# Kernel tuning notes

Hardware: AMD Instinct MI355X
Metric: run time of the kernel (lower is better)

Reference implementation:

```python
import jax, jax.numpy as jnp
import numpy as np

B, S, D_IN, D = 4, 4096, 512, 256


def setup_inputs() -> dict:
    key = jax.random.key(0)
    ks = jax.random.split(key, 7)
    return {
        "query": jax.random.normal(ks[0], (B, S, D_IN), dtype=jnp.float32),
        "key": jax.random.normal(ks[1], (B, S, D_IN), dtype=jnp.float32),
        "value": jax.random.normal(ks[2], (B, S, D), dtype=jnp.float32),
        "Wq": jax.random.normal(ks[3], (D, D_IN), dtype=jnp.float32) * (1.0 / np.sqrt(D_IN)),
        "bq": jax.random.normal(ks[4], (D,), dtype=jnp.float32) * 0.01,
        "Wk": jax.random.normal(ks[5], (D, D_IN), dtype=jnp.float32) * (1.0 / np.sqrt(D_IN)),
        "bk": jax.random.normal(ks[6], (D,), dtype=jnp.float32) * 0.01,
        "scale_factor": jnp.ones((), dtype=jnp.float32),  # source uses scale_factor = 1
        "dropout_p": 0,  # fixed to 0 -> dropout is identity (deterministic baseline)
    }


def reference(query, key, value, Wq, bq, Wk, bk, scale_factor, dropout_p):
    # q/k linear projections: [B,S,512] -> [B,S,256]
    q = jnp.einsum("bsi,di->bsd", query, Wq) + bq
    k = jnp.einsum("bsi,di->bsd", key, Wk) + bk
    # scaled dot-product attention scores [B,S,S]
    scores = jnp.einsum("bqd,bkd->bqk", q, k) * scale_factor
    attn = jax.nn.softmax(scores, axis=-1)
    # dropout_p == 0 -> identity
    out = jnp.einsum("bqk,bkd->bqd", attn, value)
    return out
```

## Files before the change

### kernel.cpp

```cpp
#include <hip/hip_runtime.h>

#define S_LEN 4096
#define NROWS 16384

typedef float f32x4 __attribute__((ext_vector_type(4)));
typedef _Float16 f16x8 __attribute__((ext_vector_type(8)));
typedef _Float16 f16x4 __attribute__((ext_vector_type(4)));

__device__ __forceinline__ unsigned short f2h(float f) {
  _Float16 h = (_Float16)f;
  return __builtin_bit_cast(unsigned short, h);
}

__device__ __forceinline__ float ex2(float x) {
  return __builtin_amdgcn_exp2f(x);
}

__device__ __forceinline__ void gload16(const void* g, void* l) {
  __builtin_amdgcn_global_load_lds(
      (const __attribute__((address_space(1))) void*)g,
      (__attribute__((address_space(3))) void*)l, 16, 0, 0);
}

__global__ void cw_kernel(const float* __restrict__ Wq, const float* __restrict__ Wk,
                          unsigned short* __restrict__ Wqb, unsigned short* __restrict__ Wkb) {
  const int i = (blockIdx.x * 256 + threadIdx.x) * 8;
  if (i >= 131072) return;
  unsigned short tmp[8] __attribute__((aligned(16)));
#pragma unroll
  for (int u = 0; u < 8; ++u) tmp[u] = f2h(Wq[i + u]);
  *(uint4*)(Wqb + i) = ((const uint4*)tmp)[0];
#pragma unroll
  for (int u = 0; u < 8; ++u) tmp[u] = f2h(Wk[i + u]);
  *(uint4*)(Wkb + i) = ((const uint4*)tmp)[0];
}

__global__ __launch_bounds__(256) void vt_kernel(const float* __restrict__ V,
                                                 unsigned short* __restrict__ Vt) {
  __shared__ float tile[64][65];
  const int tid = threadIdx.x;
  const int b = blockIdx.z, s0 = blockIdx.x * 64, d0 = blockIdx.y * 64;
  {
    const int r = tid >> 2, cs = (tid & 3) * 16;
    const float* src = V + ((long)b * S_LEN + s0 + r) * 256 + d0 + cs;
#pragma unroll
    for (int u = 0; u < 4; ++u) {
      const f32x4 v = __builtin_nontemporal_load((const f32x4*)(src + 4 * u));
      tile[r][cs + 4 * u + 0] = v[0]; tile[r][cs + 4 * u + 1] = v[1];
      tile[r][cs + 4 * u + 2] = v[2]; tile[r][cs + 4 * u + 3] = v[3];
    }
  }
  __syncthreads();
  {
    const int d = tid >> 2, ss = (tid & 3) * 16;
    unsigned short tmp[16] __attribute__((aligned(16)));
#pragma unroll
    for (int u = 0; u < 16; ++u) tmp[u] = f2h(tile[ss + u][d]);
    unsigned short* dst = Vt + ((long)b * 256 + d0 + d) * S_LEN + s0 + ss;
    *(uint4*)dst = ((const uint4*)tmp)[0];
    *((uint4*)dst + 1) = ((const uint4*)tmp)[1];
  }
}

__global__ __launch_bounds__(256, 4) void proj_kernel(
    const float* __restrict__ Xq, const float* __restrict__ Xk,
    const unsigned short* __restrict__ Wqb, const unsigned short* __restrict__ Wkb,
    const float* __restrict__ bq, const float* __restrict__ bk,
    unsigned short* __restrict__ Qb, unsigned short* __restrict__ Kb,
    const float* __restrict__ scale_ptr) {
  const int tid = threadIdx.x;
  const int lane = tid & 63, w = tid >> 6;
  const int h = lane >> 4, cc = lane & 15;
  const int z = blockIdx.y;
  const float* X = z ? Xk : Xq;
  const unsigned short* Wb = z ? Wkb : Wqb;
  const float* bias = z ? bk : bq;
  unsigned short* out = z ? Kb : Qb;
  const float sc = z ? 1.f : scale_ptr[0] * 1.44269504088896340736f;
  const int rowbase = blockIdx.x * 64;

  __shared__ char sx[8192];
  __shared__ char sw[32768];

  f32x4 acc[16];
  const f32x4 fz = {0.f, 0.f, 0.f, 0.f};
#pragma unroll
  for (int nf = 0; nf < 16; ++nf) acc[nf] = fz;

  for (int kstep = 0; kstep < 8; ++kstep) {
    const int k0 = kstep * 64;
    __syncthreads();
    {
      const int r = tid >> 2;
      const int cb0 = (tid & 3) * 2;
      const float* src = X + (long)(rowbase + r) * 512 + k0 + (tid & 3) * 16;
      float xv[16];
#pragma unroll
      for (int u = 0; u < 4; ++u) {
        const f32x4 v = __builtin_nontemporal_load((const f32x4*)(src + 4 * u));
        xv[4 * u + 0] = v[0]; xv[4 * u + 1] = v[1];
        xv[4 * u + 2] = v[2]; xv[4 * u + 3] = v[3];
      }
      unsigned short tmp[16] __attribute__((aligned(16)));
#pragma unroll
      for (int u = 0; u < 16; ++u) tmp[u] = f2h(xv[u]);
      *(uint4*)(sx + r * 128 + ((cb0 ^ (r & 7)) * 16)) = ((const uint4*)tmp)[0];
      *(uint4*)(sx + r * 128 + (((cb0 + 1) ^ (r & 7)) * 16)) = ((const uint4*)tmp)[1];
    }
#pragma unroll
    for (int i = 0; i < 8; ++i) {
      const int off = w * 8192 + i * 1024 + lane * 16;
      const int row = off >> 7;
      const int lcb = (lane & 7) ^ (row & 7);
      gload16(Wb + (long)row * 512 + k0 + lcb * 8, sw + w * 8192 + i * 1024);
    }
    __syncthreads();
#pragma unroll
    for (int ks = 0; ks < 2; ++ks) {
      const int rl = 16 * w + cc;
      const f16x8 af = *(const f16x8*)(sx + rl * 128 + (((h + 4 * ks) ^ (rl & 7)) * 16));
#pragma unroll
      for (int nf = 0; nf < 16; ++nf) {
        const int n = cc + 16 * nf;
        const f16x8 bf = *(const f16x8*)(sw + n * 128 + (((h + 4 * ks) ^ (n & 7)) * 16));
        acc[nf] = __builtin_amdgcn_mfma_f32_16x16x32_f16(af, bf, acc[nf], 0, 0, 0);
      }
    }
  }
#pragma unroll
  for (int nf = 0; nf < 16; ++nf) {
    const float bv = bias[cc + 16 * nf];
#pragma unroll
    for (int r = 0; r < 4; ++r) {
      const long grow = rowbase + 16 * w + 4 * h + r;
      out[grow * 256 + cc + 16 * nf] = f2h((acc[nf][r] + bv) * sc);
    }
  }
}

__global__ __launch_bounds__(256, 2) void attn_kernel(
    const unsigned short* __restrict__ Qb, const unsigned short* __restrict__ Kb,
    const unsigned short* __restrict__ Vt, float* __restrict__ out0,
    unsigned short* __restrict__ p16, float2* __restrict__ stats,
    int* __restrict__ cnt, int nsplit, int nchunks) {
  extern __shared__ char smem[];
  const int tid = threadIdx.x;
  const int lane = tid & 63, w = tid >> 6;
  const int h = lane >> 4, c = lane & 15;

  int* s_item_p = (int*)(smem + 69632);
  if (tid == 0) {
    const unsigned x = __builtin_amdgcn_s_getreg(6164) & 7u;
    const int pref = (int)x * nchunks / 8;
    int item = 0;
    for (int k = 0; k < nchunks; ++k) {
      const int ch = (pref + k) % nchunks;
      const int t = atomicAdd(cnt + ch, 1);
      if (t < 32) { item = ch * 32 + t; break; }
    }
    *s_item_p = item;
  }
  __syncthreads();
  const int nid = *s_item_p;
  const int gqt = nid & 255;
  const int split = nid >> 8;

  const int b = gqt >> 6;
  const int qrow0 = (gqt & 63) * 64;
  const long brow = (long)b * S_LEN;

  const int kv_len = S_LEN / nsplit;
  const int kv0 = split * kv_len;
  const int nit = kv_len / 32;

  f16x8 qf[8];
  {
    const unsigned short* qbase = Qb + (brow + qrow0 + w * 16 + c) * 256 + h * 8;
#pragma unroll
    for (int kk = 0; kk < 8; ++kk)
      qf[kk] = *(const f16x8*)(qbase + kk * 32);
  }

  f32x4 O[16];
  float mrun[4], lrun[4];
  const f32x4 fz = {0.f, 0.f, 0.f, 0.f};
#pragma unroll
  for (int nfd = 0; nfd < 16; ++nfd) O[nfd] = fz;
#pragma unroll
  for (int r = 0; r < 4; ++r) { mrun[r] = -1e30f; lrun[r] = 0.f; }

  const unsigned short* kbB = Kb + brow * 256;
  const unsigned short* vbB = Vt + (long)b * 256 * S_LEN;

  auto stage = [&](int buf, int it) {
    const int kvb = kv0 + it * 32;
#pragma unroll
    for (int i = 0; i < 4; ++i) {
      const int off = i * 4096 + tid * 16;
      {
        const int row = off >> 9;
        const int lcb = ((off >> 4) & 31) ^ (row & 7);
        gload16(kbB + (long)(kvb + row) * 256 + lcb * 8, smem + buf * 16384 + off);
      }
      {
        const int drow = off >> 6;
        const int lcb = ((off >> 4) & 3) ^ ((drow >> 1) & 3);
        gload16(vbB + (long)drow * S_LEN + kvb + lcb * 8,
                smem + 32768 + buf * 16384 + off);
      }
    }
  };

  char* const pt = smem + 65536 + w * 1024;

  stage(0, 0);
  __syncthreads();

  for (int t = 0; t < nit; ++t) {
    const int buf = t & 1;
    if (t + 1 < nit) stage(buf ^ 1, t + 1);
    const char* kt = smem + buf * 16384;
    const char* vl = smem + 32768 + buf * 16384;

    f32x4 s[2];
    s[0] = fz; s[1] = fz;
    __builtin_amdgcn_s_setprio(1);
#pragma unroll
    for (int kk = 0; kk < 8; ++kk) {
#pragma unroll
      for (int nf = 0; nf < 2; ++nf) {
        const int r = c + 16 * nf;
        const int cb = ((4 * kk + h) ^ (r & 7)) & 31;
        const f16x8 kf = *(const f16x8*)(kt + r * 512 + cb * 16);
        s[nf] = __builtin_amdgcn_mfma_f32_16x16x32_f16(qf[kk], kf, s[nf], 0, 0, 0);
      }
    }
    __builtin_amdgcn_s_setprio(0);

    {
      bool ok = true;
#pragma unroll
      for (int r = 0; r < 4; ++r)
        ok &= (fmaxf(s[0][r], s[1][r]) <= mrun[r] + 12.f);
      if (__all(ok)) {
#pragma unroll
        for (int r = 0; r < 4; ++r) {
          const float p0 = ex2(s[0][r] - mrun[r]);
          const float p1 = ex2(s[1][r] - mrun[r]);
          s[0][r] = p0; s[1][r] = p1;
          lrun[r] += p0 + p1;
        }
      } else {
#pragma unroll
        for (int r = 0; r < 4; ++r) {
          float mx = fmaxf(s[0][r], s[1][r]);
          mx = fmaxf(mx, __shfl_xor(mx, 1));
          mx = fmaxf(mx, __shfl_xor(mx, 2));
          mx = fmaxf(mx, __shfl_xor(mx, 4));
          mx = fmaxf(mx, __shfl_xor(mx, 8));
          const float mnew = fmaxf(mrun[r], mx);
          const float alpha = ex2(mrun[r] - mnew);
          const float p0 = ex2(s[0][r] - mnew);
          const float p1 = ex2(s[1][r] - mnew);
          s[0][r] = p0; s[1][r] = p1;
          lrun[r] = lrun[r] * alpha + p0 + p1;
          mrun[r] = mnew;
#pragma unroll
          for (int nfd = 0; nfd < 16; ++nfd) O[nfd][r] *= alpha;
        }
      }
#pragma unroll
      for (int nf = 0; nf < 2; ++nf)
#pragma unroll
        for (int r = 0; r < 4; ++r) {
          const int C = c + 16 * nf;
          const int blk = ((C >> 3) ^ r ^ h) & 3;
          *(unsigned short*)(pt + (4 * h + r) * 64 + blk * 16 + (C & 7) * 2) =
              f2h(s[nf][r]);
        }
    }
    asm volatile("" ::: "memory");

    __builtin_amdgcn_s_setprio(1);
    {
      const f16x8 pa = *(const f16x8*)(pt + c * 64 + (((h ^ c ^ (c >> 2)) & 3) * 16));
#pragma unroll
      for (int nfd = 0; nfd < 16; ++nfd) {
        const int dr = c + 16 * nfd;
        const f16x8 vf = *(const f16x8*)(vl + dr * 64 + (((h ^ (dr >> 1)) & 3) * 16));
        O[nfd] = __builtin_amdgcn_mfma_f32_16x16x32_f16(pa, vf, O[nfd], 0, 0, 0);
      }
    }
    __builtin_amdgcn_s_setprio(0);
    __syncthreads();
  }

#pragma unroll
  for (int r = 0; r < 4; ++r) {
    float l = lrun[r];
    l += __shfl_xor(l, 1); l += __shfl_xor(l, 2);
    l += __shfl_xor(l, 4); l += __shfl_xor(l, 8);
    lrun[r] = l;
  }

  const long rowg0 = brow + qrow0 + w * 16 + 4 * h;
  float inv[4];
#pragma unroll
  for (int r = 0; r < 4; ++r) inv[r] = 1.f / lrun[r];

  if (nsplit == 1) {
#pragma unroll
    for (int nfd = 0; nfd < 16; ++nfd)
#pragma unroll
      for (int r = 0; r < 4; ++r)
        out0[(rowg0 + r) * 256 + c + 16 * nfd] = O[nfd][r] * inv[r];
  } else {
    unsigned short* dst = p16 + (long)split * NROWS * 256;
#pragma unroll
    for (int nfd = 0; nfd < 16; ++nfd)
#pragma unroll
      for (int r = 0; r < 4; ++r)
        dst[(rowg0 + r) * 256 + c + 16 * nfd] = f2h(O[nfd][r] * inv[r]);
    if (c == 0) {
#pragma unroll
      for (int r = 0; r < 4; ++r)
        stats[(long)split * NROWS + rowg0 + r] = make_float2(mrun[r], lrun[r]);
    }
  }
}

__global__ __launch_bounds__(256) void merge_kernel(float* __restrict__ out0,
                                                    const unsigned short* __restrict__ p16,
                                                    const float2* __restrict__ stats,
                                                    int nsplit) {
  const int i4 = blockIdx.x * 256 + threadIdx.x;
  const int row = i4 >> 6;
  float2 st[4];
#pragma unroll
  for (int s = 0; s < 4; ++s)
    st[s] = (s < nsplit) ? stats[s * NROWS + row] : make_float2(-1e30f, 0.f);
  const float m = fmaxf(fmaxf(st[0].x, st[1].x), fmaxf(st[2].x, st[3].x));
  float wgt[4], den = 0.f;
#pragma unroll
  for (int s = 0; s < 4; ++s) {
    wgt[s] = st[s].y * __builtin_amdgcn_exp2f(st[s].x - m);
    den += wgt[s];
  }
  const float invd = 1.f / den;
  float ax = 0.f, ay = 0.f, az = 0.f, aw = 0.f;
#pragma unroll
  for (int s = 0; s < 4; ++s) {
    if (s < nsplit) {
      const f16x4 v = ((const f16x4*)(p16 + (long)s * NROWS * 256))[i4];
      ax += (float)v[0] * wgt[s]; ay += (float)v[1] * wgt[s];
      az += (float)v[2] * wgt[s]; aw += (float)v[3] * wgt[s];
    }
  }
  const f32x4 res = {ax * invd, ay * invd, az * invd, aw * invd};
  ((f32x4*)out0)[i4] = res;
}

extern "C" void kernel_launch(void* const* d_in, const int* in_sizes, int n_in,
                              void* d_out, int out_size, void* d_ws, size_t ws_size,
                              hipStream_t stream) {
  const float* query = (const float*)d_in[0];
  const float* key   = (const float*)d_in[1];
  const float* value = (const float*)d_in[2];
  const float* Wq    = (const float*)d_in[3];
  const float* bq    = (const float*)d_in[4];
  const float* Wk    = (const float*)d_in[5];
  const float* bk    = (const float*)d_in[6];
  const float* scale = (const float*)d_in[7];
  float* out = (float*)d_out;

  char* ws = (char*)d_ws;
  unsigned short* Wqb = (unsigned short*)(ws);
  unsigned short* Wkb = (unsigned short*)(ws + 262144);
  unsigned short* Qb  = (unsigned short*)(ws + 524288);
  unsigned short* Kb  = (unsigned short*)(ws + 8912896);
  unsigned short* Vt  = (unsigned short*)(ws + 17301504);
  int* cnt            = (int*)(ws + 25690112);
  float2* stats       = (float2*)(ws + 25694208);
  unsigned short* p16 = (unsigned short*)(ws + 26218496);

  int nsplit = 1;
  if (ws_size >= 42995712) nsplit = 2;
  const int nblk = 256 * nsplit;
  const int nchunks = nblk / 32;

  hipMemsetAsync(cnt, 0, 64, stream);
  cw_kernel<<<64, 256, 0, stream>>>(Wq, Wk, Wqb, Wkb);
  vt_kernel<<<dim3(64, 4, 4), 256, 0, stream>>>(value, Vt);
  proj_kernel<<<dim3(256, 2), 256, 0, stream>>>(query, key, Wqb, Wkb, bq, bk, Qb, Kb, scale);

  hipFuncSetAttribute((const void*)attn_kernel,
                      hipFuncAttributeMaxDynamicSharedMemorySize, 69648);
  attn_kernel<<<nblk, 256, 69648, stream>>>(Qb, Kb, Vt, out, p16,
                                            stats, cnt, nsplit, nchunks);
  if (nsplit > 1)
    merge_kernel<<<4096, 256, 0, stream>>>(out, p16, stats, nsplit);
}
```

Measured before the change: 182.7 us.

## Merge V transpose into projection kernel and batch LDS loads before MFMAs

The V transpose/convert kernel is folded into the Q/K projection kernel as extra blocks (block index >= 512), so one launch covers both and the two kinds of blocks can run at the same time. In the attention loop, all K and V fragment reads from LDS are now issued before the MFMA chains instead of interleaved with them, to hide LDS latency. The batched fragments need more registers, which could lower occupancy or cause spills. The V-transpose blocks now also reserve the projection's larger shared-memory allocation.

```diff
diff --git a/kernel.cpp b/kernel.cpp
--- a/kernel.cpp
+++ b/kernel.cpp
@@ -35,52 +35,55 @@
   *(uint4*)(Wkb + i) = ((const uint4*)tmp)[0];
 }
 
-__global__ __launch_bounds__(256) void vt_kernel(const float* __restrict__ V,
-                                                 unsigned short* __restrict__ Vt) {
-  __shared__ float tile[64][65];
-  const int tid = threadIdx.x;
-  const int b = blockIdx.z, s0 = blockIdx.x * 64, d0 = blockIdx.y * 64;
-  {
-    const int r = tid >> 2, cs = (tid & 3) * 16;
-    const float* src = V + ((long)b * S_LEN + s0 + r) * 256 + d0 + cs;
-#pragma unroll
-    for (int u = 0; u < 4; ++u) {
-      const f32x4 v = __builtin_nontemporal_load((const f32x4*)(src + 4 * u));
-      tile[r][cs + 4 * u + 0] = v[0]; tile[r][cs + 4 * u + 1] = v[1];
-      tile[r][cs + 4 * u + 2] = v[2]; tile[r][cs + 4 * u + 3] = v[3];
-    }
-  }
-  __syncthreads();
-  {
-    const int d = tid >> 2, ss = (tid & 3) * 16;
-    unsigned short tmp[16] __attribute__((aligned(16)));
-#pragma unroll
-    for (int u = 0; u < 16; ++u) tmp[u] = f2h(tile[ss + u][d]);
-    unsigned short* dst = Vt + ((long)b * 256 + d0 + d) * S_LEN + s0 + ss;
-    *(uint4*)dst = ((const uint4*)tmp)[0];
-    *((uint4*)dst + 1) = ((const uint4*)tmp)[1];
-  }
-}
-
-__global__ __launch_bounds__(256, 4) void proj_kernel(
+__global__ __launch_bounds__(256, 4) void prep_kernel(
     const float* __restrict__ Xq, const float* __restrict__ Xk,
     const unsigned short* __restrict__ Wqb, const unsigned short* __restrict__ Wkb,
     const float* __restrict__ bq, const float* __restrict__ bk,
     unsigned short* __restrict__ Qb, unsigned short* __restrict__ Kb,
-    const float* __restrict__ scale_ptr) {
+    const float* __restrict__ scale_ptr,
+    const float* __restrict__ V, unsigned short* __restrict__ Vt) {
+  __shared__ char shm[40960];
   const int tid = threadIdx.x;
+
+  if (blockIdx.x >= 512) {
+    const int vid = blockIdx.x - 512;
+    const int b = vid >> 8, d0 = ((vid >> 6) & 3) * 64, s0 = (vid & 63) * 64;
+    float (*tile)[65] = (float(*)[65])shm;
+    {
+      const int r = tid >> 2, cs = (tid & 3) * 16;
+      const float* src = V + ((long)b * S_LEN + s0 + r) * 256 + d0 + cs;
+#pragma unroll
+      for (int u = 0; u < 4; ++u) {
+        const f32x4 v = __builtin_nontemporal_load((const f32x4*)(src + 4 * u));
+        tile[r][cs + 4 * u + 0] = v[0]; tile[r][cs + 4 * u + 1] = v[1];
+        tile[r][cs + 4 * u + 2] = v[2]; tile[r][cs + 4 * u + 3] = v[3];
+      }
+    }
+    __syncthreads();
+    {
+      const int d = tid >> 2, ss = (tid & 3) * 16;
+      unsigned short tmp[16] __attribute__((aligned(16)));
+#pragma unroll
+      for (int u = 0; u < 16; ++u) tmp[u] = f2h(tile[ss + u][d]);
+      unsigned short* dst = Vt + ((long)b * 256 + d0 + d) * S_LEN + s0 + ss;
+      *(uint4*)dst = ((const uint4*)tmp)[0];
+      *((uint4*)dst + 1) = ((const uint4*)tmp)[1];
+    }
+    return;
+  }
+
+  const int z = blockIdx.x & 1;
+  const int rowbase = (blockIdx.x >> 1) * 64;
   const int lane = tid & 63, w = tid >> 6;
   const int h = lane >> 4, cc = lane & 15;
-  const int z = blockIdx.y;
   const float* X = z ? Xk : Xq;
   const unsigned short* Wb = z ? Wkb : Wqb;
   const float* bias = z ? bk : bq;
   unsigned short* out = z ? Kb : Qb;
   const float sc = z ? 1.f : scale_ptr[0] * 1.44269504088896340736f;
-  const int rowbase = blockIdx.x * 64;
-
-  __shared__ char sx[8192];
-  __shared__ char sw[32768];
+
+  char* const sx = shm;
+  char* const sw = shm + 8192;
 
   f32x4 acc[16];
   const f32x4 fz = {0.f, 0.f, 0.f, 0.f};
@@ -224,18 +227,23 @@
 
     f32x4 s[2];
     s[0] = fz; s[1] = fz;
-    __builtin_amdgcn_s_setprio(1);
-#pragma unroll
-    for (int kk = 0; kk < 8; ++kk) {
-#pragma unroll
-      for (int nf = 0; nf < 2; ++nf) {
-        const int r = c + 16 * nf;
-        const int cb = ((4 * kk + h) ^ (r & 7)) & 31;
-        const f16x8 kf = *(const f16x8*)(kt + r * 512 + cb * 16);
-        s[nf] = __builtin_amdgcn_mfma_f32_16x16x32_f16(qf[kk], kf, s[nf], 0, 0, 0);
-      }
-    }
-    __builtin_amdgcn_s_setprio(0);
+    {
+      f16x8 kfa[8], kfb[8];
+#pragma unroll
+      for (int kk = 0; kk < 8; ++kk) {
+        const int cb = ((4 * kk + h) ^ (c & 7)) & 31;
+        kfa[kk] = *(const f16x8*)(kt + c * 512 + cb * 16);
+        kfb[kk] = *(const f16x8*)(kt + (c + 16) * 512 + cb * 16);
+      }
+      __builtin_amdgcn_s_setprio(1);
+#pragma unroll
+      for (int kk = 0; kk < 8; ++kk)
+        s[0] = __builtin_amdgcn_mfma_f32_16x16x32_f16(qf[kk], kfa[kk], s[0], 0, 0, 0);
+#pragma unroll
+      for (int kk = 0; kk < 8; ++kk)
+        s[1] = __builtin_amdgcn_mfma_f32_16x16x32_f16(qf[kk], kfb[kk], s[1], 0, 0, 0);
+      __builtin_amdgcn_s_setprio(0);
+    }
 
     {
       bool ok = true;
@@ -284,12 +292,24 @@
     __builtin_amdgcn_s_setprio(1);
     {
       const f16x8 pa = *(const f16x8*)(pt + c * 64 + (((h ^ c ^ (c >> 2)) & 3) * 16));
-#pragma unroll
-      for (int nfd = 0; nfd < 16; ++nfd) {
-        const int dr = c + 16 * nfd;
-        const f16x8 vf = *(const f16x8*)(vl + dr * 64 + (((h ^ (dr >> 1)) & 3) * 16));
-        O[nfd] = __builtin_amdgcn_mfma_f32_16x16x32_f16(pa, vf, O[nfd], 0, 0, 0);
-      }
+      f16x8 vfa[8];
+#pragma unroll
+      for (int i = 0; i < 8; ++i) {
+        const int dr = c + 16 * i;
+        vfa[i] = *(const f16x8*)(vl + dr * 64 + (((h ^ (dr >> 1)) & 3) * 16));
+      }
+      f16x8 vfb[8];
+#pragma unroll
+      for (int i = 0; i < 8; ++i) {
+        const int dr = c + 16 * (i + 8);
+        vfb[i] = *(const f16x8*)(vl + dr * 64 + (((h ^ (dr >> 1)) & 3) * 16));
+      }
+#pragma unroll
+      for (int i = 0; i < 8; ++i)
+        O[i] = __builtin_amdgcn_mfma_f32_16x16x32_f16(pa, vfa[i], O[i], 0, 0, 0);
+#pragma unroll
+      for (int i = 0; i < 8; ++i)
+        O[i + 8] = __builtin_amdgcn_mfma_f32_16x16x32_f16(pa, vfb[i], O[i + 8], 0, 0, 0);
     }
     __builtin_amdgcn_s_setprio(0);
     __syncthreads();
@@ -390,9 +410,8 @@
 
   hipMemsetAsync(cnt, 0, 64, stream);
   cw_kernel<<<64, 256, 0, stream>>>(Wq, Wk, Wqb, Wkb);
-  vt_kernel<<<dim3(64, 4, 4), 256, 0, stream>>>(value, Vt);
-  proj_kernel<<<dim3(256, 2), 256, 0, stream>>>(query, key, Wqb, Wkb, bq, bk, Qb, Kb, scale);
-
+  prep_kernel<<<1536, 256, 0, stream>>>(query, key, Wqb, Wkb, bq, bk, Qb, Kb,
+                                        scale, value, Vt);
   hipFuncSetAttribute((const void*)attn_kernel,
                       hipFuncAttributeMaxDynamicSharedMemorySize, 69648);
   attn_kernel<<<nblk, 256, 69648, stream>>>(Qb, Kb, Vt, out, p16,
```

Result: no change. 183.8 us (+0.6%).
